# Kernel optimization log

Hardware: AMD Instinct MI355X
Metric: run time of the kernel (lower is better)

The kernel has to match this reference:

```python
import jax, jax.numpy as jnp
import numpy as np

NUM_NODES = 50000
NUM_EDGES = 800000
NUM_LABEL_EDGES = 100000
F_IN, F_HID, F_OUT = 128, 128, 64


def gcn_conv(x, src, dst, W, b, n):
    # PyG GCNConv: h = x @ W; add self-loops; symmetric normalization
    # deg counted on destination (col), including self-loop (+1).
    h = x @ W
    deg = jax.ops.segment_sum(jnp.ones(src.shape, h.dtype), dst, num_segments=n) + 1.0
    dinv = jax.lax.rsqrt(deg)  # deg >= 1 always (self-loop)
    norm = dinv[src] * dinv[dst]                       # [E]
    agg = jax.ops.segment_sum(h[src] * norm[:, None], dst, num_segments=n)
    agg = agg + h * (dinv * dinv)[:, None]             # self-loop term dinv[i]^2 * h[i]
    return agg + b


def setup_inputs() -> dict:
    key = jax.random.key(0)
    ks = jax.random.split(key, 9)
    x = jax.random.normal(ks[0], (NUM_NODES, F_IN), dtype=jnp.float32)
    edge_index = jax.random.randint(ks[1], (2, NUM_EDGES), 0, NUM_NODES, dtype=jnp.int64)
    edge_label_index = jax.random.randint(ks[2], (2, NUM_LABEL_EDGES), 0, NUM_NODES, dtype=jnp.int64)
    def glorot(k, fi, fo):
        s = (6.0 / (fi + fo)) ** 0.5
        return jax.random.uniform(k, (fi, fo), jnp.float32, -s, s)
    return {
        "x": x,
        "edge_index": edge_index,
        "edge_label_index": edge_label_index,
        "W1": glorot(ks[3], F_IN, F_HID),  "b1": jnp.zeros((F_HID,), jnp.float32),
        "W2": glorot(ks[4], F_HID, F_HID), "b2": jnp.zeros((F_HID,), jnp.float32),
        "W3": glorot(ks[5], F_HID, F_OUT), "b3": jnp.zeros((F_OUT,), jnp.float32),
    }


def reference(x, edge_index, edge_label_index, W1, b1, W2, b2, W3, b3):
    src, dst = edge_index[0], edge_index[1]
    z = jax.nn.relu(gcn_conv(x, src, dst, W1, b1, NUM_NODES))
    z = jax.nn.relu(gcn_conv(z, src, dst, W2, b2, NUM_NODES))
    z = gcn_conv(z, src, dst, W3, b3, NUM_NODES)
    # decode: dot product of endpoint embeddings per label edge
    return jnp.sum(z[edge_label_index[0]] * z[edge_label_index[1]], axis=-1)
```

## Files before the change

kernel.cpp:

```cpp
#include <hip/hip_runtime.h>
#include <hip/hip_bf16.h>
#include <stdint.h>

#define NN 50000
#define NE 800000
#define NL 100000
#define F_IN 128
#define F_HID 128
#define F_OUT 64
#define SLOTS 64

#define NB 196
#define BSH 8
#define BCAP 5376

typedef __attribute__((ext_vector_type(8))) short bf16x8;
typedef __attribute__((ext_vector_type(4))) float f32x4;
typedef __attribute__((ext_vector_type(4))) unsigned int u32x4;

__device__ __forceinline__ float asf(unsigned int u) {
    union { unsigned int i; float f; } c; c.i = u; return c.f;
}
__device__ __forceinline__ float bflo(unsigned int x) { return asf(x << 16); }
__device__ __forceinline__ float bfhi(unsigned int x) { return asf(x & 0xffff0000u); }
__device__ __forceinline__ unsigned short f2bf(float f) {
    union { float f; unsigned int i; } c; c.f = f;
    unsigned int u = c.i + (0x7fffu + ((c.i >> 16) & 1u));
    return (unsigned short)(u >> 16);
}


__global__ void wprep(const float* __restrict__ W1, const float* __restrict__ W2,
                      const float* __restrict__ W3, unsigned short* __restrict__ Wt,
                      int* __restrict__ cursor) {
    if (blockIdx.x == 0 && threadIdx.x < NB) cursor[threadIdx.x] = 0;
    int idx = blockIdx.x * 256 + threadIdx.x;
    const float* W; unsigned short* O; int base, Mloc;
    if (idx < 16384)      { W = W1; O = Wt;         base = idx;         Mloc = 128; }
    else if (idx < 32768) { W = W2; O = Wt + 16384; base = idx - 16384; Mloc = 128; }
    else                  { W = W3; O = Wt + 32768; base = idx - 32768; Mloc = 64;  }
    int n = base >> 7, k = base & 127;
    O[base] = f2bf(W[k * Mloc + n]);
}


__global__ __launch_bounds__(256) void bin_edges(
        const int* __restrict__ src, const int* __restrict__ dst,
        int* __restrict__ cursor, unsigned int* __restrict__ binbuf) {
    __shared__ int hcnt[NB];
    __shared__ int hbase[NB];
    int tid = threadIdx.x;
    if (tid < NB) hcnt[tid] = 0;
    __syncthreads();
    int e0 = blockIdx.x * 2048;
#pragma unroll
    for (int r = 0; r < 8; ++r) {
        int e = e0 + r * 256 + tid;
        if (e < NE) atomicAdd(&hcnt[dst[e] >> BSH], 1);
    }
    __syncthreads();
    if (tid < NB) { hbase[tid] = atomicAdd(&cursor[tid], hcnt[tid]); hcnt[tid] = 0; }
    __syncthreads();
#pragma unroll
    for (int r = 0; r < 8; ++r) {
        int e = e0 + r * 256 + tid;
        if (e < NE) {
            int d = dst[e], s = src[e];
            int b = d >> BSH;
            int p = hbase[b] + atomicAdd(&hcnt[b], 1);
            if (p < BCAP)
                __builtin_nontemporal_store(
                    (unsigned int)s | ((unsigned int)d << 16),
                    &binbuf[(size_t)b * BCAP + p]);
        }
    }
}


__global__ __launch_bounds__(256) void build_csr(
        const unsigned int* __restrict__ binbuf, const int* __restrict__ cursor,
        int* __restrict__ deg, unsigned short* __restrict__ colp) {
    __shared__ unsigned short lcol[256 * SLOTS];
    __shared__ int ldeg[256];
    int tid = threadIdx.x;
    int blk = blockIdx.x;
    int base = blk << BSH;
    int nNodes = min(256, NN - base);
    ldeg[tid] = 0;
    __syncthreads();
    int cnt = min(cursor[blk], BCAP);
    for (int e = tid; e < cnt; e += 256) {
        unsigned int pk = __builtin_nontemporal_load(&binbuf[(size_t)blk * BCAP + e]);
        int d = (int)(pk >> 16) - base;
        int p = atomicAdd(&ldeg[d], 1);
        if (p < SLOTS) lcol[d * SLOTS + p] = (unsigned short)(pk & 0xffffu);
    }
    __syncthreads();
    if (tid < nNodes) deg[base + tid] = ldeg[tid];
    u32x4* gout = (u32x4*)(colp + (size_t)base * SLOTS);
    const u32x4* lin = (const u32x4*)lcol;
    for (int i = tid; i < nNodes * 8; i += 256) gout[i] = lin[i];
}


template <int M_, int AFP32>
__global__ __launch_bounds__(256) void gemm_mfma(
        const void* __restrict__ Av, const unsigned short* __restrict__ Wt,
        const int* __restrict__ deg, unsigned short* __restrict__ Outb, int N) {
    constexpr int K = 128;
    constexpr int NT = M_ / 16;
    int lane = threadIdx.x & 63;
    int wave = threadIdx.x >> 6;
    int m    = lane & 15;
    int quad = lane >> 4;
    int rowA = blockIdx.x * 64 + wave * 16 + m;
    int rA   = min(rowA, N - 1);

    bf16x8 afr[4];
    if (AFP32) {
        const float* A = (const float*)Av;
        const float* p = A + (size_t)rA * K + quad * 8;
#pragma unroll
        for (int s = 0; s < 4; ++s) {
            float4 lo = *(const float4*)(p + s * 32);
            float4 hi = *(const float4*)(p + s * 32 + 4);
            bf16x8 r;
            r[0] = (short)f2bf(lo.x); r[1] = (short)f2bf(lo.y);
            r[2] = (short)f2bf(lo.z); r[3] = (short)f2bf(lo.w);
            r[4] = (short)f2bf(hi.x); r[5] = (short)f2bf(hi.y);
            r[6] = (short)f2bf(hi.z); r[7] = (short)f2bf(hi.w);
            afr[s] = r;
        }
    } else {
        const unsigned short* A = (const unsigned short*)Av;
#pragma unroll
        for (int s = 0; s < 4; ++s)
            afr[s] = *(const bf16x8*)(A + (size_t)rA * K + s * 32 + quad * 8);
    }

    f32x4 acc[NT];
#pragma unroll
    for (int t = 0; t < NT; ++t) { acc[t][0] = 0.f; acc[t][1] = 0.f; acc[t][2] = 0.f; acc[t][3] = 0.f; }

#pragma unroll
    for (int t = 0; t < NT; ++t) {
        const unsigned short* wp = Wt + (size_t)(t * 16 + m) * K + quad * 8;
#pragma unroll
        for (int s = 0; s < 4; ++s) {
            bf16x8 bfr = *(const bf16x8*)(wp + s * 32);
            acc[t] = __builtin_amdgcn_mfma_f32_16x16x32_bf16(afr[s], bfr, acc[t], 0, 0, 0);
        }
    }

    int outRowBase = blockIdx.x * 64 + wave * 16 + quad * 4;
    float di[4];
#pragma unroll
    for (int i = 0; i < 4; ++i) {
        int rr = min(outRowBase + i, N - 1);
        di[i] = rsqrtf((float)deg[rr] + 1.0f);
    }
#pragma unroll
    for (int t = 0; t < NT; ++t) {
#pragma unroll
        for (int i = 0; i < 4; ++i) {
            int rr = outRowBase + i;
            if (rr < N)
                Outb[(size_t)rr * M_ + t * 16 + m] = f2bf(acc[t][i] * di[i]);
        }
    }
}


template <int F, int RELU>
__global__ __launch_bounds__(256) void aggregate(
        const unsigned short* __restrict__ hs, const int* __restrict__ deg,
        const unsigned short* __restrict__ colp, const float* __restrict__ bias,
        unsigned short* __restrict__ out, int n) {
    int wave = threadIdx.x >> 6;
    int lane = threadIdx.x & 63;
    int node = blockIdx.x * 4 + wave;
    if (node >= n) return;

    float acc0 = 0.f, acc1 = 0.f;
    if (F == 128) {
        unsigned int v = *(const unsigned int*)(hs + (size_t)node * F + lane * 2);
        acc0 = bflo(v); acc1 = bfhi(v);
    } else {
        acc0 = bflo((unsigned int)hs[(size_t)node * F + lane]);
    }

    int cnt = min(deg[node], SLOTS);
    int myIdx = (lane < cnt) ? (int)colp[(size_t)node * SLOTS + lane] : 0;
    for (int j = 0; j < cnt; j += 8) {
        int iv[8]; unsigned int mk[8];
#pragma unroll
        for (int u = 0; u < 8; ++u) {
            iv[u] = __shfl(myIdx, j + u, 64);
            mk[u] = (j + u < cnt) ? 0xffffffffu : 0u;
        }
        if (F == 128) {
            unsigned int vv[8];
#pragma unroll
            for (int u = 0; u < 8; ++u)
                vv[u] = *(const unsigned int*)(hs + (size_t)iv[u] * F + lane * 2);
#pragma unroll
            for (int u = 0; u < 8; ++u) {
                unsigned int x = vv[u] & mk[u];
                acc0 += bflo(x); acc1 += bfhi(x);
            }
        } else {
            unsigned short vv[8];
#pragma unroll
            for (int u = 0; u < 8; ++u)
                vv[u] = hs[(size_t)iv[u] * F + lane];
#pragma unroll
            for (int u = 0; u < 8; ++u)
                acc0 += bflo(((unsigned int)vv[u]) & mk[u]);
        }
    }

    float di = rsqrtf((float)deg[node] + 1.0f);
    if (F == 128) {
        float o0 = di * acc0 + bias[lane * 2];
        float o1 = di * acc1 + bias[lane * 2 + 1];
        if (RELU) { o0 = fmaxf(o0, 0.f); o1 = fmaxf(o1, 0.f); }
        unsigned int w = (unsigned int)f2bf(o0) | ((unsigned int)f2bf(o1) << 16);
        *(unsigned int*)(out + (size_t)node * F + lane * 2) = w;
    } else {
        float o = di * acc0 + bias[lane];
        if (RELU) o = fmaxf(o, 0.f);
        out[(size_t)node * F + lane] = f2bf(o);
    }
}


__global__ __launch_bounds__(256) void decode(
        const unsigned short* __restrict__ z, const int* __restrict__ ls,
        const int* __restrict__ ld, float* __restrict__ out, int nl) {
    int wave = threadIdx.x >> 6;
    int lane = threadIdx.x & 63;
    int e = blockIdx.x * 4 + wave;
    if (e >= nl) return;
    float p = bflo((unsigned int)z[(size_t)ls[e] * F_OUT + lane]) *
              bflo((unsigned int)z[(size_t)ld[e] * F_OUT + lane]);
#pragma unroll
    for (int off = 32; off > 0; off >>= 1) p += __shfl_down(p, off, 64);
    if (lane == 0) out[e] = p;
}


static inline size_t align256(size_t x) { return (x + 255) & ~(size_t)255; }

extern "C" void kernel_launch(void* const* d_in, const int* in_sizes, int n_in,
                              void* d_out, int out_size, void* d_ws, size_t ws_size,
                              hipStream_t stream) {
    const float* x  = (const float*)d_in[0];
    const int*   ei = (const int*)d_in[1];
    const int*   li = (const int*)d_in[2];
    const float* W1 = (const float*)d_in[3];
    const float* b1 = (const float*)d_in[4];
    const float* W2 = (const float*)d_in[5];
    const float* b2 = (const float*)d_in[6];
    const float* W3 = (const float*)d_in[7];
    const float* b3 = (const float*)d_in[8];
    float* out = (float*)d_out;

    const int* src = ei;
    const int* dst = ei + NE;
    const int* ls = li;
    const int* ld = li + NL;

    char* ws = (char*)d_ws;
    size_t off = 0;
    int* deg    = (int*)(ws + off); off += align256(NN * 4);
    int* cursor = (int*)(ws + off); off += align256(NB * 4);
    unsigned int* binbuf = (unsigned int*)(ws + off); off += align256((size_t)NB * BCAP * 4);
    unsigned short* colp = (unsigned short*)(ws + off); off += align256((size_t)NN * SLOTS * 2);
    unsigned short* Wtb  = (unsigned short*)(ws + off); off += align256(40960 * 2);
    unsigned short* bufH = (unsigned short*)(ws + off); off += align256((size_t)NN * F_HID * 2);
    unsigned short* bufP = (unsigned short*)(ws + off); off += align256((size_t)NN * F_HID * 2);

    const int aggBlocks = (NN + 3) / 4;
    const int gemmBlocks = (NN + 63) / 64;
    const int binBlocks = (NE + 2047) / 2048;

    wprep<<<160, 256, 0, stream>>>(W1, W2, W3, Wtb, cursor);
    bin_edges<<<binBlocks, 256, 0, stream>>>(src, dst, cursor, binbuf);
    build_csr<<<NB, 256, 0, stream>>>(binbuf, cursor, deg, colp);

    gemm_mfma<128, 1><<<gemmBlocks, 256, 0, stream>>>(x, Wtb, deg, bufH, NN);
    aggregate<128, 1><<<aggBlocks, 256, 0, stream>>>(bufH, deg, colp, b1, bufP, NN);

    gemm_mfma<128, 0><<<gemmBlocks, 256, 0, stream>>>(bufP, Wtb + 16384, deg, bufH, NN);
    aggregate<128, 1><<<aggBlocks, 256, 0, stream>>>(bufH, deg, colp, b2, bufP, NN);

    gemm_mfma<64, 0><<<gemmBlocks, 256, 0, stream>>>(bufP, Wtb + 32768, deg, bufH, NN);
    aggregate<64, 0><<<aggBlocks, 256, 0, stream>>>(bufH, deg, colp, b3, bufP, NN);

    decode<<<(NL + 3) / 4, 256, 0, stream>>>(bufP, ls, ld, out, NL);
}
```

Measured before the change: 273.0 us.

## Fuse all stages into one persistent cooperative kernel with grid syncs

Replaces the ten separate kernel launches with a single cooperative persistent kernel. The kernel runs each stage (weight prep, edge binning, CSR build, three GEMM and aggregate pairs, decode) as grid-strided phases separated by grid.sync. The aim is to remove per-launch overhead and inter-kernel gaps. In exchange, each grid-wide barrier has a cost, occupancy is capped at 1024 blocks, and the phases lose the latency hiding that very large launches gave the aggregate stage. A fallback path with separate launches is kept for when the cooperative launch fails.

```diff
diff --git a/kernel.cpp b/kernel.cpp
--- a/kernel.cpp
+++ b/kernel.cpp
@@ -1,13 +1,13 @@
 #include <hip/hip_runtime.h>
+#include <hip/hip_cooperative_groups.h>
 #include <hip/hip_bf16.h>
 #include <stdint.h>
+
+namespace cg = cooperative_groups;
 
 #define NN 50000
 #define NE 800000
 #define NL 100000
-#define F_IN 128
-#define F_HID 128
-#define F_OUT 64
 #define SLOTS 64
 
 #define NB 196
@@ -30,222 +30,312 @@
 }
 
 
-__global__ void wprep(const float* __restrict__ W1, const float* __restrict__ W2,
-                      const float* __restrict__ W3, unsigned short* __restrict__ Wt,
-                      int* __restrict__ cursor) {
-    if (blockIdx.x == 0 && threadIdx.x < NB) cursor[threadIdx.x] = 0;
-    int idx = blockIdx.x * 256 + threadIdx.x;
-    const float* W; unsigned short* O; int base, Mloc;
-    if (idx < 16384)      { W = W1; O = Wt;         base = idx;         Mloc = 128; }
-    else if (idx < 32768) { W = W2; O = Wt + 16384; base = idx - 16384; Mloc = 128; }
-    else                  { W = W3; O = Wt + 32768; base = idx - 32768; Mloc = 64;  }
-    int n = base >> 7, k = base & 127;
-    O[base] = f2bf(W[k * Mloc + n]);
-}
-
-
-__global__ __launch_bounds__(256) void bin_edges(
+__device__ __forceinline__ void wprep_phase(
+        const float* __restrict__ W1, const float* __restrict__ W2,
+        const float* __restrict__ W3, unsigned short* __restrict__ Wt,
+        int* __restrict__ cursor) {
+    for (int idx = blockIdx.x * 256 + threadIdx.x; idx < 40960;
+         idx += gridDim.x * 256) {
+        if (idx < NB) cursor[idx] = 0;
+        const float* W; unsigned short* O; int base, Mloc;
+        if (idx < 16384)      { W = W1; O = Wt;         base = idx;         Mloc = 128; }
+        else if (idx < 32768) { W = W2; O = Wt + 16384; base = idx - 16384; Mloc = 128; }
+        else                  { W = W3; O = Wt + 32768; base = idx - 32768; Mloc = 64;  }
+        int n = base >> 7, k = base & 127;
+        O[base] = f2bf(W[k * Mloc + n]);
+    }
+}
+
+__device__ __forceinline__ void bin_phase(
+        const int* __restrict__ src, const int* __restrict__ dst,
+        int* __restrict__ cursor, unsigned int* __restrict__ binbuf,
+        int* hcnt, int* hbase) {
+    int tid = threadIdx.x;
+    if (tid < NB) hcnt[tid] = 0;
+    __syncthreads();
+    int chunk = (NE + gridDim.x - 1) / gridDim.x;
+    int e0 = blockIdx.x * chunk;
+    int e1 = min(e0 + chunk, NE);
+    for (int e = e0 + tid; e < e1; e += 256)
+        atomicAdd(&hcnt[dst[e] >> BSH], 1);
+    __syncthreads();
+    if (tid < NB) { hbase[tid] = atomicAdd(&cursor[tid], hcnt[tid]); hcnt[tid] = 0; }
+    __syncthreads();
+    for (int e = e0 + tid; e < e1; e += 256) {
+        int d = dst[e], s = src[e];
+        int b = d >> BSH;
+        int p = hbase[b] + atomicAdd(&hcnt[b], 1);
+        if (p < BCAP)
+            __builtin_nontemporal_store(
+                (unsigned int)s | ((unsigned int)d << 16),
+                &binbuf[(size_t)b * BCAP + p]);
+    }
+}
+
+__device__ __forceinline__ void csr_phase(
+        const unsigned int* __restrict__ binbuf, const int* __restrict__ cursor,
+        int* __restrict__ deg, unsigned short* __restrict__ colp,
+        unsigned short* lcol, int* ldeg) {
+    int tid = threadIdx.x;
+    for (int blk = blockIdx.x; blk < NB; blk += gridDim.x) {
+        int base = blk << BSH;
+        int nNodes = min(256, NN - base);
+        ldeg[tid] = 0;
+        __syncthreads();
+        int cnt = min(cursor[blk], BCAP);
+        for (int e = tid; e < cnt; e += 256) {
+            unsigned int pk = __builtin_nontemporal_load(&binbuf[(size_t)blk * BCAP + e]);
+            int d = (int)(pk >> 16) - base;
+            int p = atomicAdd(&ldeg[d], 1);
+            if (p < SLOTS) lcol[d * SLOTS + p] = (unsigned short)(pk & 0xffffu);
+        }
+        __syncthreads();
+        if (tid < nNodes) deg[base + tid] = ldeg[tid];
+        u32x4* gout = (u32x4*)(colp + (size_t)base * SLOTS);
+        const u32x4* lin = (const u32x4*)lcol;
+        for (int i = tid; i < nNodes * 8; i += 256) gout[i] = lin[i];
+        __syncthreads();
+    }
+}
+
+template <int M_, int AFP32>
+__device__ __forceinline__ void gemm_phase(
+        const void* __restrict__ Av, const unsigned short* __restrict__ Wt,
+        const int* __restrict__ deg, unsigned short* __restrict__ Outb, int N) {
+    constexpr int K = 128;
+    constexpr int NT = M_ / 16;
+    int tid = threadIdx.x;
+    int lane = tid & 63;
+    int wave = tid >> 6;
+    int m    = lane & 15;
+    int quad = lane >> 4;
+    const int VB = (NN + 63) / 64;
+    for (int vb = blockIdx.x; vb < VB; vb += gridDim.x) {
+        int rowA = vb * 64 + wave * 16 + m;
+        int rA   = min(rowA, N - 1);
+
+        bf16x8 afr[4];
+        if (AFP32) {
+            const float* A = (const float*)Av;
+            const float* p = A + (size_t)rA * K + quad * 8;
+#pragma unroll
+            for (int s = 0; s < 4; ++s) {
+                float4 lo = *(const float4*)(p + s * 32);
+                float4 hi = *(const float4*)(p + s * 32 + 4);
+                bf16x8 r;
+                r[0] = (short)f2bf(lo.x); r[1] = (short)f2bf(lo.y);
+                r[2] = (short)f2bf(lo.z); r[3] = (short)f2bf(lo.w);
+                r[4] = (short)f2bf(hi.x); r[5] = (short)f2bf(hi.y);
+                r[6] = (short)f2bf(hi.z); r[7] = (short)f2bf(hi.w);
+                afr[s] = r;
+            }
+        } else {
+            const unsigned short* A = (const unsigned short*)Av;
+#pragma unroll
+            for (int s = 0; s < 4; ++s)
+                afr[s] = *(const bf16x8*)(A + (size_t)rA * K + s * 32 + quad * 8);
+        }
+
+        f32x4 acc[NT];
+#pragma unroll
+        for (int t = 0; t < NT; ++t) { acc[t][0] = 0.f; acc[t][1] = 0.f; acc[t][2] = 0.f; acc[t][3] = 0.f; }
+
+#pragma unroll
+        for (int t = 0; t < NT; ++t) {
+            const unsigned short* wp = Wt + (size_t)(t * 16 + m) * K + quad * 8;
+#pragma unroll
+            for (int s = 0; s < 4; ++s) {
+                bf16x8 bfr = *(const bf16x8*)(wp + s * 32);
+                acc[t] = __builtin_amdgcn_mfma_f32_16x16x32_bf16(afr[s], bfr, acc[t], 0, 0, 0);
+            }
+        }
+
+        int outRowBase = vb * 64 + wave * 16 + quad * 4;
+        float di[4];
+#pragma unroll
+        for (int i = 0; i < 4; ++i) {
+            int rr = min(outRowBase + i, N - 1);
+            di[i] = rsqrtf((float)deg[rr] + 1.0f);
+        }
+#pragma unroll
+        for (int t = 0; t < NT; ++t) {
+#pragma unroll
+            for (int i = 0; i < 4; ++i) {
+                int rr = outRowBase + i;
+                if (rr < N)
+                    Outb[(size_t)rr * M_ + t * 16 + m] = f2bf(acc[t][i] * di[i]);
+            }
+        }
+    }
+}
+
+template <int F, int RELU>
+__device__ __forceinline__ void agg_phase(
+        const unsigned short* __restrict__ hs, const int* __restrict__ deg,
+        const unsigned short* __restrict__ colp, const float* __restrict__ bias,
+        unsigned short* __restrict__ out, int n) {
+    int tid = threadIdx.x;
+    int wave = tid >> 6;
+    int lane = tid & 63;
+    const int VB = (NN + 3) / 4;
+    for (int vb = blockIdx.x; vb < VB; vb += gridDim.x) {
+        int node = vb * 4 + wave;
+        if (node >= n) continue;
+
+        float acc0 = 0.f, acc1 = 0.f;
+        if (F == 128) {
+            unsigned int v = *(const unsigned int*)(hs + (size_t)node * F + lane * 2);
+            acc0 = bflo(v); acc1 = bfhi(v);
+        } else {
+            acc0 = bflo((unsigned int)hs[(size_t)node * F + lane]);
+        }
+
+        int cnt = min(deg[node], SLOTS);
+        int myIdx = (lane < cnt) ? (int)colp[(size_t)node * SLOTS + lane] : 0;
+        for (int j = 0; j < cnt; j += 8) {
+            int iv[8]; unsigned int mk[8];
+#pragma unroll
+            for (int u = 0; u < 8; ++u) {
+                iv[u] = __shfl(myIdx, j + u, 64);
+                mk[u] = (j + u < cnt) ? 0xffffffffu : 0u;
+            }
+            if (F == 128) {
+                unsigned int vv[8];
+#pragma unroll
+                for (int u = 0; u < 8; ++u)
+                    vv[u] = *(const unsigned int*)(hs + (size_t)iv[u] * F + lane * 2);
+#pragma unroll
+                for (int u = 0; u < 8; ++u) {
+                    unsigned int xv = vv[u] & mk[u];
+                    acc0 += bflo(xv); acc1 += bfhi(xv);
+                }
+            } else {
+                unsigned short vv[8];
+#pragma unroll
+                for (int u = 0; u < 8; ++u)
+                    vv[u] = hs[(size_t)iv[u] * F + lane];
+#pragma unroll
+                for (int u = 0; u < 8; ++u)
+                    acc0 += bflo(((unsigned int)vv[u]) & mk[u]);
+            }
+        }
+
+        float di = rsqrtf((float)deg[node] + 1.0f);
+        if (F == 128) {
+            float o0 = di * acc0 + bias[lane * 2];
+            float o1 = di * acc1 + bias[lane * 2 + 1];
+            if (RELU) { o0 = fmaxf(o0, 0.f); o1 = fmaxf(o1, 0.f); }
+            unsigned int w = (unsigned int)f2bf(o0) | ((unsigned int)f2bf(o1) << 16);
+            *(unsigned int*)(out + (size_t)node * F + lane * 2) = w;
+        } else {
+            float o = di * acc0 + bias[lane];
+            if (RELU) o = fmaxf(o, 0.f);
+            out[(size_t)node * F + lane] = f2bf(o);
+        }
+    }
+}
+
+__device__ __forceinline__ void decode_phase(
+        const unsigned short* __restrict__ z, const int* __restrict__ ls,
+        const int* __restrict__ ld, float* __restrict__ out) {
+    int tid = threadIdx.x;
+    int wave = tid >> 6;
+    int lane = tid & 63;
+    const int VB = (NL + 3) / 4;
+    for (int vb = blockIdx.x; vb < VB; vb += gridDim.x) {
+        int e = vb * 4 + wave;
+        if (e >= NL) continue;
+        float p = bflo((unsigned int)z[(size_t)ls[e] * 64 + lane]) *
+                  bflo((unsigned int)z[(size_t)ld[e] * 64 + lane]);
+#pragma unroll
+        for (int off = 32; off > 0; off >>= 1) p += __shfl_down(p, off, 64);
+        if (lane == 0) out[e] = p;
+    }
+}
+
+
+__global__ __launch_bounds__(256, 4) void fused(
+        const float* __restrict__ x, const int* __restrict__ ei,
+        const int* __restrict__ li,
+        const float* __restrict__ W1, const float* __restrict__ b1,
+        const float* __restrict__ W2, const float* __restrict__ b2,
+        const float* __restrict__ W3, const float* __restrict__ b3,
+        float* __restrict__ out,
+        int* __restrict__ deg, int* __restrict__ cursor,
+        unsigned int* __restrict__ binbuf, unsigned short* __restrict__ colp,
+        unsigned short* __restrict__ Wtb, unsigned short* __restrict__ bufH,
+        unsigned short* __restrict__ bufP) {
+    cg::grid_group grid = cg::this_grid();
+    __shared__ __align__(16) char smem[33792];
+    const int* src = ei;
+    const int* dst = ei + NE;
+
+    wprep_phase(W1, W2, W3, Wtb, cursor);
+    grid.sync();
+    bin_phase(src, dst, cursor, binbuf, (int*)smem, (int*)smem + NB);
+    grid.sync();
+    csr_phase(binbuf, cursor, deg, colp,
+              (unsigned short*)smem, (int*)(smem + 32768));
+    grid.sync();
+
+    gemm_phase<128, 1>(x, Wtb, deg, bufH, NN);
+    grid.sync();
+    agg_phase<128, 1>(bufH, deg, colp, b1, bufP, NN);
+    grid.sync();
+    gemm_phase<128, 0>(bufP, Wtb + 16384, deg, bufH, NN);
+    grid.sync();
+    agg_phase<128, 1>(bufH, deg, colp, b2, bufP, NN);
+    grid.sync();
+    gemm_phase<64, 0>(bufP, Wtb + 32768, deg, bufH, NN);
+    grid.sync();
+    agg_phase<64, 0>(bufH, deg, colp, b3, bufP, NN);
+    grid.sync();
+
+    decode_phase(bufP, li, li + NL, out);
+}
+
+
+__global__ void k_wprep(const float* __restrict__ W1, const float* __restrict__ W2,
+                        const float* __restrict__ W3, unsigned short* __restrict__ Wt,
+                        int* __restrict__ cursor) {
+    wprep_phase(W1, W2, W3, Wt, cursor);
+}
+
+__global__ __launch_bounds__(256) void k_bin(
         const int* __restrict__ src, const int* __restrict__ dst,
         int* __restrict__ cursor, unsigned int* __restrict__ binbuf) {
     __shared__ int hcnt[NB];
     __shared__ int hbase[NB];
-    int tid = threadIdx.x;
-    if (tid < NB) hcnt[tid] = 0;
-    __syncthreads();
-    int e0 = blockIdx.x * 2048;
-#pragma unroll
-    for (int r = 0; r < 8; ++r) {
-        int e = e0 + r * 256 + tid;
-        if (e < NE) atomicAdd(&hcnt[dst[e] >> BSH], 1);
-    }
-    __syncthreads();
-    if (tid < NB) { hbase[tid] = atomicAdd(&cursor[tid], hcnt[tid]); hcnt[tid] = 0; }
-    __syncthreads();
-#pragma unroll
-    for (int r = 0; r < 8; ++r) {
-        int e = e0 + r * 256 + tid;
-        if (e < NE) {
-            int d = dst[e], s = src[e];
-            int b = d >> BSH;
-            int p = hbase[b] + atomicAdd(&hcnt[b], 1);
-            if (p < BCAP)
-                __builtin_nontemporal_store(
-                    (unsigned int)s | ((unsigned int)d << 16),
-                    &binbuf[(size_t)b * BCAP + p]);
-        }
-    }
-}
-
-
-__global__ __launch_bounds__(256) void build_csr(
+    bin_phase(src, dst, cursor, binbuf, hcnt, hbase);
+}
+
+__global__ __launch_bounds__(256) void k_csr(
         const unsigned int* __restrict__ binbuf, const int* __restrict__ cursor,
         int* __restrict__ deg, unsigned short* __restrict__ colp) {
     __shared__ unsigned short lcol[256 * SLOTS];
     __shared__ int ldeg[256];
-    int tid = threadIdx.x;
-    int blk = blockIdx.x;
-    int base = blk << BSH;
-    int nNodes = min(256, NN - base);
-    ldeg[tid] = 0;
-    __syncthreads();
-    int cnt = min(cursor[blk], BCAP);
-    for (int e = tid; e < cnt; e += 256) {
-        unsigned int pk = __builtin_nontemporal_load(&binbuf[(size_t)blk * BCAP + e]);
-        int d = (int)(pk >> 16) - base;
-        int p = atomicAdd(&ldeg[d], 1);
-        if (p < SLOTS) lcol[d * SLOTS + p] = (unsigned short)(pk & 0xffffu);
-    }
-    __syncthreads();
-    if (tid < nNodes) deg[base + tid] = ldeg[tid];
-    u32x4* gout = (u32x4*)(colp + (size_t)base * SLOTS);
-    const u32x4* lin = (const u32x4*)lcol;
-    for (int i = tid; i < nNodes * 8; i += 256) gout[i] = lin[i];
-}
-
+    csr_phase(binbuf, cursor, deg, colp, lcol, ldeg);
+}
 
 template <int M_, int AFP32>
-__global__ __launch_bounds__(256) void gemm_mfma(
+__global__ __launch_bounds__(256) void k_gemm(
         const void* __restrict__ Av, const unsigned short* __restrict__ Wt,
         const int* __restrict__ deg, unsigned short* __restrict__ Outb, int N) {
-    constexpr int K = 128;
-    constexpr int NT = M_ / 16;
-    int lane = threadIdx.x & 63;
-    int wave = threadIdx.x >> 6;
-    int m    = lane & 15;
-    int quad = lane >> 4;
-    int rowA = blockIdx.x * 64 + wave * 16 + m;
-    int rA   = min(rowA, N - 1);
-
-    bf16x8 afr[4];
-    if (AFP32) {
-        const float* A = (const float*)Av;
-        const float* p = A + (size_t)rA * K + quad * 8;
-#pragma unroll
-        for (int s = 0; s < 4; ++s) {
-            float4 lo = *(const float4*)(p + s * 32);
-            float4 hi = *(const float4*)(p + s * 32 + 4);
-            bf16x8 r;
-            r[0] = (short)f2bf(lo.x); r[1] = (short)f2bf(lo.y);
-            r[2] = (short)f2bf(lo.z); r[3] = (short)f2bf(lo.w);
-            r[4] = (short)f2bf(hi.x); r[5] = (short)f2bf(hi.y);
-            r[6] = (short)f2bf(hi.z); r[7] = (short)f2bf(hi.w);
-            afr[s] = r;
-        }
-    } else {
-        const unsigned short* A = (const unsigned short*)Av;
-#pragma unroll
-        for (int s = 0; s < 4; ++s)
-            afr[s] = *(const bf16x8*)(A + (size_t)rA * K + s * 32 + quad * 8);
-    }
-
-    f32x4 acc[NT];
-#pragma unroll
-    for (int t = 0; t < NT; ++t) { acc[t][0] = 0.f; acc[t][1] = 0.f; acc[t][2] = 0.f; acc[t][3] = 0.f; }
-
-#pragma unroll
-    for (int t = 0; t < NT; ++t) {
-        const unsigned short* wp = Wt + (size_t)(t * 16 + m) * K + quad * 8;
-#pragma unroll
-        for (int s = 0; s < 4; ++s) {
-            bf16x8 bfr = *(const bf16x8*)(wp + s * 32);
-            acc[t] = __builtin_amdgcn_mfma_f32_16x16x32_bf16(afr[s], bfr, acc[t], 0, 0, 0);
-        }
-    }
-
-    int outRowBase = blockIdx.x * 64 + wave * 16 + quad * 4;
-    float di[4];
-#pragma unroll
-    for (int i = 0; i < 4; ++i) {
-        int rr = min(outRowBase + i, N - 1);
-        di[i] = rsqrtf((float)deg[rr] + 1.0f);
-    }
-#pragma unroll
-    for (int t = 0; t < NT; ++t) {
-#pragma unroll
-        for (int i = 0; i < 4; ++i) {
-            int rr = outRowBase + i;
-            if (rr < N)
-                Outb[(size_t)rr * M_ + t * 16 + m] = f2bf(acc[t][i] * di[i]);
-        }
-    }
-}
-
+    gemm_phase<M_, AFP32>(Av, Wt, deg, Outb, N);
+}
 
 template <int F, int RELU>
-__global__ __launch_bounds__(256) void aggregate(
+__global__ __launch_bounds__(256) void k_agg(
         const unsigned short* __restrict__ hs, const int* __restrict__ deg,
         const unsigned short* __restrict__ colp, const float* __restrict__ bias,
         unsigned short* __restrict__ out, int n) {
-    int wave = threadIdx.x >> 6;
-    int lane = threadIdx.x & 63;
-    int node = blockIdx.x * 4 + wave;
-    if (node >= n) return;
-
-    float acc0 = 0.f, acc1 = 0.f;
-    if (F == 128) {
-        unsigned int v = *(const unsigned int*)(hs + (size_t)node * F + lane * 2);
-        acc0 = bflo(v); acc1 = bfhi(v);
-    } else {
-        acc0 = bflo((unsigned int)hs[(size_t)node * F + lane]);
-    }
-
-    int cnt = min(deg[node], SLOTS);
-    int myIdx = (lane < cnt) ? (int)colp[(size_t)node * SLOTS + lane] : 0;
-    for (int j = 0; j < cnt; j += 8) {
-        int iv[8]; unsigned int mk[8];
-#pragma unroll
-        for (int u = 0; u < 8; ++u) {
-            iv[u] = __shfl(myIdx, j + u, 64);
-            mk[u] = (j + u < cnt) ? 0xffffffffu : 0u;
-        }
-        if (F == 128) {
-            unsigned int vv[8];
-#pragma unroll
-            for (int u = 0; u < 8; ++u)
-                vv[u] = *(const unsigned int*)(hs + (size_t)iv[u] * F + lane * 2);
-#pragma unroll
-            for (int u = 0; u < 8; ++u) {
-                unsigned int x = vv[u] & mk[u];
-                acc0 += bflo(x); acc1 += bfhi(x);
-            }
-        } else {
-            unsigned short vv[8];
-#pragma unroll
-            for (int u = 0; u < 8; ++u)
-                vv[u] = hs[(size_t)iv[u] * F + lane];
-#pragma unroll
-            for (int u = 0; u < 8; ++u)
-                acc0 += bflo(((unsigned int)vv[u]) & mk[u]);
-        }
-    }
-
-    float di = rsqrtf((float)deg[node] + 1.0f);
-    if (F == 128) {
-        float o0 = di * acc0 + bias[lane * 2];
-        float o1 = di * acc1 + bias[lane * 2 + 1];
-        if (RELU) { o0 = fmaxf(o0, 0.f); o1 = fmaxf(o1, 0.f); }
-        unsigned int w = (unsigned int)f2bf(o0) | ((unsigned int)f2bf(o1) << 16);
-        *(unsigned int*)(out + (size_t)node * F + lane * 2) = w;
-    } else {
-        float o = di * acc0 + bias[lane];
-        if (RELU) o = fmaxf(o, 0.f);
-        out[(size_t)node * F + lane] = f2bf(o);
-    }
-}
-
-
-__global__ __launch_bounds__(256) void decode(
+    agg_phase<F, RELU>(hs, deg, colp, bias, out, n);
+}
+
+__global__ __launch_bounds__(256) void k_decode(
         const unsigned short* __restrict__ z, const int* __restrict__ ls,
-        const int* __restrict__ ld, float* __restrict__ out, int nl) {
-    int wave = threadIdx.x >> 6;
-    int lane = threadIdx.x & 63;
-    int e = blockIdx.x * 4 + wave;
-    if (e >= nl) return;
-    float p = bflo((unsigned int)z[(size_t)ls[e] * F_OUT + lane]) *
-              bflo((unsigned int)z[(size_t)ld[e] * F_OUT + lane]);
-#pragma unroll
-    for (int off = 32; off > 0; off >>= 1) p += __shfl_down(p, off, 64);
-    if (lane == 0) out[e] = p;
+        const int* __restrict__ ld, float* __restrict__ out) {
+    decode_phase(z, ls, ld, out);
 }
 
 
@@ -265,11 +355,6 @@
     const float* b3 = (const float*)d_in[8];
     float* out = (float*)d_out;
 
-    const int* src = ei;
-    const int* dst = ei + NE;
-    const int* ls = li;
-    const int* ld = li + NL;
-
     char* ws = (char*)d_ws;
     size_t off = 0;
     int* deg    = (int*)(ws + off); off += align256(NN * 4);
@@ -277,25 +362,39 @@
     unsigned int* binbuf = (unsigned int*)(ws + off); off += align256((size_t)NB * BCAP * 4);
     unsigned short* colp = (unsigned short*)(ws + off); off += align256((size_t)NN * SLOTS * 2);
     unsigned short* Wtb  = (unsigned short*)(ws + off); off += align256(40960 * 2);
-    unsigned short* bufH = (unsigned short*)(ws + off); off += align256((size_t)NN * F_HID * 2);
-    unsigned short* bufP = (unsigned short*)(ws + off); off += align256((size_t)NN * F_HID * 2);
-
-    const int aggBlocks = (NN + 3) / 4;
-    const int gemmBlocks = (NN + 63) / 64;
-    const int binBlocks = (NE + 2047) / 2048;
-
-    wprep<<<160, 256, 0, stream>>>(W1, W2, W3, Wtb, cursor);
-    bin_edges<<<binBlocks, 256, 0, stream>>>(src, dst, cursor, binbuf);
-    build_csr<<<NB, 256, 0, stream>>>(binbuf, cursor, deg, colp);
-
-    gemm_mfma<128, 1><<<gemmBlocks, 256, 0, stream>>>(x, Wtb, deg, bufH, NN);
-    aggregate<128, 1><<<aggBlocks, 256, 0, stream>>>(bufH, deg, colp, b1, bufP, NN);
-
-    gemm_mfma<128, 0><<<gemmBlocks, 256, 0, stream>>>(bufP, Wtb + 16384, deg, bufH, NN);
-    aggregate<128, 1><<<aggBlocks, 256, 0, stream>>>(bufH, deg, colp, b2, bufP, NN);
-
-    gemm_mfma<64, 0><<<gemmBlocks, 256, 0, stream>>>(bufP, Wtb + 32768, deg, bufH, NN);
-    aggregate<64, 0><<<aggBlocks, 256, 0, stream>>>(bufH, deg, colp, b3, bufP, NN);
-
-    decode<<<(NL + 3) / 4, 256, 0, stream>>>(bufP, ls, ld, out, NL);
-}
+    unsigned short* bufH = (unsigned short*)(ws + off); off += align256((size_t)NN * 128 * 2);
+    unsigned short* bufP = (unsigned short*)(ws + off); off += align256((size_t)NN * 128 * 2);
+
+    int perCU = 0;
+    hipError_t oe = hipOccupancyMaxActiveBlocksPerMultiprocessor(&perCU, fused, 256, 0);
+    bool coop_ok = false;
+    if (oe == hipSuccess && perCU > 0) {
+        int grid = perCU * 256;
+        if (grid > 1024) grid = 1024;
+        void* kargs[] = {
+            (void*)&x, (void*)&ei, (void*)&li,
+            (void*)&W1, (void*)&b1, (void*)&W2, (void*)&b2, (void*)&W3, (void*)&b3,
+            (void*)&out,
+            (void*)&deg, (void*)&cursor, (void*)&binbuf, (void*)&colp,
+            (void*)&Wtb, (void*)&bufH, (void*)&bufP
+        };
+        hipError_t le = hipLaunchCooperativeKernel((const void*)fused, dim3(grid),
+                                                   dim3(256), kargs, 0, stream);
+        coop_ok = (le == hipSuccess);
+    }
+
+    if (!coop_ok) {
+        const int* src = ei;
+        const int* dst = ei + NE;
+        k_wprep<<<160, 256, 0, stream>>>(W1, W2, W3, Wtb, cursor);
+        k_bin<<<391, 256, 0, stream>>>(src, dst, cursor, binbuf);
+        k_csr<<<NB, 256, 0, stream>>>(binbuf, cursor, deg, colp);
+        k_gemm<128, 1><<<782, 256, 0, stream>>>(x, Wtb, deg, bufH, NN);
+        k_agg<128, 1><<<12500, 256, 0, stream>>>(bufH, deg, colp, b1, bufP, NN);
+        k_gemm<128, 0><<<782, 256, 0, stream>>>(bufP, Wtb + 16384, deg, bufH, NN);
+        k_agg<128, 1><<<12500, 256, 0, stream>>>(bufH, deg, colp, b2, bufP, NN);
+        k_gemm<64, 0><<<782, 256, 0, stream>>>(bufP, Wtb + 32768, deg, bufH, NN);
+        k_agg<64, 0><<<12500, 256, 0, stream>>>(bufH, deg, colp, b3, bufP, NN);
+        k_decode<<<25000, 256, 0, stream>>>(bufP, li, li + NL, out);
+    }
+}
```

New measurement: 931.1 us. 241% more time.

## Fuse aggregation of layers 1-2 with the following GEMM via LDS tiles

Applied to the files above, without the earlier changes.

Each block of the new kernel aggregates 16 nodes' neighbor features, applies bias, ReLU and normalization, and stages the bf16 rows in shared memory. The block then runs the next layer's MFMA GEMM on that tile directly. This removes two global write/read round trips of the hidden activations and two kernel launches. In exchange each block covers only 16 rows and reloads the full weight matrix from cache, which lowers GEMM efficiency. Other edits are renames and specialization of templates into fixed kernels.

```diff
diff --git a/kernel.cpp b/kernel.cpp
--- a/kernel.cpp
+++ b/kernel.cpp
@@ -5,9 +5,6 @@
 #define NN 50000
 #define NE 800000
 #define NL 100000
-#define F_IN 128
-#define F_HID 128
-#define F_OUT 64
 #define SLOTS 64
 
 #define NB 196
@@ -29,12 +26,11 @@
     return (unsigned short)(u >> 16);
 }
 
-
-__global__ void wprep(const float* __restrict__ W1, const float* __restrict__ W2,
-                      const float* __restrict__ W3, unsigned short* __restrict__ Wt,
-                      int* __restrict__ cursor) {
-    if (blockIdx.x == 0 && threadIdx.x < NB) cursor[threadIdx.x] = 0;
+__global__ void k_wprep(const float* __restrict__ W1, const float* __restrict__ W2,
+                        const float* __restrict__ W3, unsigned short* __restrict__ Wt,
+                        int* __restrict__ cursor) {
     int idx = blockIdx.x * 256 + threadIdx.x;
+    if (idx < NB) cursor[idx] = 0;
     const float* W; unsigned short* O; int base, Mloc;
     if (idx < 16384)      { W = W1; O = Wt;         base = idx;         Mloc = 128; }
     else if (idx < 32768) { W = W2; O = Wt + 16384; base = idx - 16384; Mloc = 128; }
@@ -43,8 +39,7 @@
     O[base] = f2bf(W[k * Mloc + n]);
 }
 
-
-__global__ __launch_bounds__(256) void bin_edges(
+__global__ __launch_bounds__(256) void k_bin(
         const int* __restrict__ src, const int* __restrict__ dst,
         int* __restrict__ cursor, unsigned int* __restrict__ binbuf) {
     __shared__ int hcnt[NB];
@@ -53,31 +48,24 @@
     if (tid < NB) hcnt[tid] = 0;
     __syncthreads();
     int e0 = blockIdx.x * 2048;
-#pragma unroll
-    for (int r = 0; r < 8; ++r) {
-        int e = e0 + r * 256 + tid;
-        if (e < NE) atomicAdd(&hcnt[dst[e] >> BSH], 1);
-    }
+    int e1 = min(e0 + 2048, NE);
+    for (int e = e0 + tid; e < e1; e += 256)
+        atomicAdd(&hcnt[dst[e] >> BSH], 1);
     __syncthreads();
     if (tid < NB) { hbase[tid] = atomicAdd(&cursor[tid], hcnt[tid]); hcnt[tid] = 0; }
     __syncthreads();
-#pragma unroll
-    for (int r = 0; r < 8; ++r) {
-        int e = e0 + r * 256 + tid;
-        if (e < NE) {
-            int d = dst[e], s = src[e];
-            int b = d >> BSH;
-            int p = hbase[b] + atomicAdd(&hcnt[b], 1);
-            if (p < BCAP)
-                __builtin_nontemporal_store(
-                    (unsigned int)s | ((unsigned int)d << 16),
-                    &binbuf[(size_t)b * BCAP + p]);
-        }
-    }
-}
-
-
-__global__ __launch_bounds__(256) void build_csr(
+    for (int e = e0 + tid; e < e1; e += 256) {
+        int d = dst[e], s = src[e];
+        int b = d >> BSH;
+        int p = hbase[b] + atomicAdd(&hcnt[b], 1);
+        if (p < BCAP)
+            __builtin_nontemporal_store(
+                (unsigned int)s | ((unsigned int)d << 16),
+                &binbuf[(size_t)b * BCAP + p]);
+    }
+}
+
+__global__ __launch_bounds__(256) void k_csr(
         const unsigned int* __restrict__ binbuf, const int* __restrict__ cursor,
         int* __restrict__ deg, unsigned short* __restrict__ colp) {
     __shared__ unsigned short lcol[256 * SLOTS];
@@ -102,46 +90,34 @@
     for (int i = tid; i < nNodes * 8; i += 256) gout[i] = lin[i];
 }
 
-
-template <int M_, int AFP32>
-__global__ __launch_bounds__(256) void gemm_mfma(
-        const void* __restrict__ Av, const unsigned short* __restrict__ Wt,
+__global__ __launch_bounds__(256) void k_gemm1(
+        const float* __restrict__ A, const unsigned short* __restrict__ Wt,
         const int* __restrict__ deg, unsigned short* __restrict__ Outb, int N) {
     constexpr int K = 128;
-    constexpr int NT = M_ / 16;
-    int lane = threadIdx.x & 63;
-    int wave = threadIdx.x >> 6;
-    int m    = lane & 15;
-    int quad = lane >> 4;
+    constexpr int NT = 8;
+    int tid = threadIdx.x;
+    int lane = tid & 63, wave = tid >> 6;
+    int m = lane & 15, quad = lane >> 4;
     int rowA = blockIdx.x * 64 + wave * 16 + m;
-    int rA   = min(rowA, N - 1);
+    int rA = min(rowA, N - 1);
 
     bf16x8 afr[4];
-    if (AFP32) {
-        const float* A = (const float*)Av;
-        const float* p = A + (size_t)rA * K + quad * 8;
-#pragma unroll
-        for (int s = 0; s < 4; ++s) {
-            float4 lo = *(const float4*)(p + s * 32);
-            float4 hi = *(const float4*)(p + s * 32 + 4);
-            bf16x8 r;
-            r[0] = (short)f2bf(lo.x); r[1] = (short)f2bf(lo.y);
-            r[2] = (short)f2bf(lo.z); r[3] = (short)f2bf(lo.w);
-            r[4] = (short)f2bf(hi.x); r[5] = (short)f2bf(hi.y);
-            r[6] = (short)f2bf(hi.z); r[7] = (short)f2bf(hi.w);
-            afr[s] = r;
-        }
-    } else {
-        const unsigned short* A = (const unsigned short*)Av;
-#pragma unroll
-        for (int s = 0; s < 4; ++s)
-            afr[s] = *(const bf16x8*)(A + (size_t)rA * K + s * 32 + quad * 8);
+    const float* p = A + (size_t)rA * K + quad * 8;
+#pragma unroll
+    for (int s = 0; s < 4; ++s) {
+        float4 lo = *(const float4*)(p + s * 32);
+        float4 hi = *(const float4*)(p + s * 32 + 4);
+        bf16x8 r;
+        r[0] = (short)f2bf(lo.x); r[1] = (short)f2bf(lo.y);
+        r[2] = (short)f2bf(lo.z); r[3] = (short)f2bf(lo.w);
+        r[4] = (short)f2bf(hi.x); r[5] = (short)f2bf(hi.y);
+        r[6] = (short)f2bf(hi.z); r[7] = (short)f2bf(hi.w);
+        afr[s] = r;
     }
 
     f32x4 acc[NT];
 #pragma unroll
     for (int t = 0; t < NT; ++t) { acc[t][0] = 0.f; acc[t][1] = 0.f; acc[t][2] = 0.f; acc[t][3] = 0.f; }
-
 #pragma unroll
     for (int t = 0; t < NT; ++t) {
         const unsigned short* wp = Wt + (size_t)(t * 16 + m) * K + quad * 8;
@@ -155,40 +131,105 @@
     int outRowBase = blockIdx.x * 64 + wave * 16 + quad * 4;
     float di[4];
 #pragma unroll
-    for (int i = 0; i < 4; ++i) {
-        int rr = min(outRowBase + i, N - 1);
-        di[i] = rsqrtf((float)deg[rr] + 1.0f);
-    }
-#pragma unroll
-    for (int t = 0; t < NT; ++t) {
+    for (int i = 0; i < 4; ++i) di[i] = rsqrtf((float)deg[min(outRowBase + i, N - 1)] + 1.0f);
+#pragma unroll
+    for (int t = 0; t < NT; ++t)
 #pragma unroll
         for (int i = 0; i < 4; ++i) {
             int rr = outRowBase + i;
-            if (rr < N)
-                Outb[(size_t)rr * M_ + t * 16 + m] = f2bf(acc[t][i] * di[i]);
-        }
-    }
-}
-
-
-template <int F, int RELU>
-__global__ __launch_bounds__(256) void aggregate(
+            if (rr < N) Outb[(size_t)rr * 128 + t * 16 + m] = f2bf(acc[t][i] * di[i]);
+        }
+}
+
+template <int M_>
+__global__ __launch_bounds__(256) void k_agg_gemm(
+        const unsigned short* __restrict__ hs, const int* __restrict__ deg,
+        const unsigned short* __restrict__ colp, const float* __restrict__ bias,
+        const unsigned short* __restrict__ Wt, unsigned short* __restrict__ Outb) {
+    constexpr int K = 128;
+    constexpr int NT = M_ / 64;
+    __shared__ unsigned short As[16][132];
+    int tid = threadIdx.x;
+    int lane = tid & 63, wave = tid >> 6;
+    int tileBase = blockIdx.x * 16;
+
+#pragma unroll
+    for (int t = 0; t < 4; ++t) {
+        int r = wave * 4 + t;
+        int node = tileBase + r;
+        unsigned int v = *(const unsigned int*)(hs + (size_t)node * K + lane * 2);
+        float acc0 = bflo(v), acc1 = bfhi(v);
+
+        int cnt = min(deg[node], SLOTS);
+        int myIdx = (lane < cnt) ? (int)colp[(size_t)node * SLOTS + lane] : 0;
+        for (int j = 0; j < cnt; j += 8) {
+            int iv[8]; unsigned int mk[8];
+#pragma unroll
+            for (int u = 0; u < 8; ++u) {
+                iv[u] = __shfl(myIdx, j + u, 64);
+                mk[u] = (j + u < cnt) ? 0xffffffffu : 0u;
+            }
+            unsigned int vv[8];
+#pragma unroll
+            for (int u = 0; u < 8; ++u)
+                vv[u] = *(const unsigned int*)(hs + (size_t)iv[u] * K + lane * 2);
+#pragma unroll
+            for (int u = 0; u < 8; ++u) {
+                unsigned int xv = vv[u] & mk[u];
+                acc0 += bflo(xv); acc1 += bfhi(xv);
+            }
+        }
+        float di = rsqrtf((float)deg[node] + 1.0f);
+        float o0 = fmaxf(di * acc0 + bias[lane * 2], 0.f);
+        float o1 = fmaxf(di * acc1 + bias[lane * 2 + 1], 0.f);
+        *(unsigned int*)&As[r][lane * 2] =
+            (unsigned int)f2bf(o0) | ((unsigned int)f2bf(o1) << 16);
+    }
+    __syncthreads();
+
+    int m = lane & 15, quad = lane >> 4;
+    bf16x8 afr[4];
+#pragma unroll
+    for (int s = 0; s < 4; ++s)
+        afr[s] = *(const bf16x8*)&As[m][s * 32 + quad * 8];
+
+    f32x4 acc[NT];
+#pragma unroll
+    for (int t = 0; t < NT; ++t) { acc[t][0] = 0.f; acc[t][1] = 0.f; acc[t][2] = 0.f; acc[t][3] = 0.f; }
+#pragma unroll
+    for (int t = 0; t < NT; ++t) {
+        int ct = wave * NT + t;
+        const unsigned short* wp = Wt + (size_t)(ct * 16 + m) * K + quad * 8;
+#pragma unroll
+        for (int s = 0; s < 4; ++s) {
+            bf16x8 bfr = *(const bf16x8*)(wp + s * 32);
+            acc[t] = __builtin_amdgcn_mfma_f32_16x16x32_bf16(afr[s], bfr, acc[t], 0, 0, 0);
+        }
+    }
+
+    int rowBase = tileBase + quad * 4;
+    float di[4];
+#pragma unroll
+    for (int i = 0; i < 4; ++i) di[i] = rsqrtf((float)deg[rowBase + i] + 1.0f);
+#pragma unroll
+    for (int t = 0; t < NT; ++t) {
+        int ct = wave * NT + t;
+#pragma unroll
+        for (int i = 0; i < 4; ++i)
+            Outb[(size_t)(rowBase + i) * M_ + ct * 16 + m] = f2bf(acc[t][i] * di[i]);
+    }
+}
+
+__global__ __launch_bounds__(256) void k_agg64(
         const unsigned short* __restrict__ hs, const int* __restrict__ deg,
         const unsigned short* __restrict__ colp, const float* __restrict__ bias,
         unsigned short* __restrict__ out, int n) {
-    int wave = threadIdx.x >> 6;
-    int lane = threadIdx.x & 63;
+    int tid = threadIdx.x;
+    int wave = tid >> 6, lane = tid & 63;
     int node = blockIdx.x * 4 + wave;
     if (node >= n) return;
 
-    float acc0 = 0.f, acc1 = 0.f;
-    if (F == 128) {
-        unsigned int v = *(const unsigned int*)(hs + (size_t)node * F + lane * 2);
-        acc0 = bflo(v); acc1 = bfhi(v);
-    } else {
-        acc0 = bflo((unsigned int)hs[(size_t)node * F + lane]);
-    }
-
+    float acc0 = bflo((unsigned int)hs[(size_t)node * 64 + lane]);
     int cnt = min(deg[node], SLOTS);
     int myIdx = (lane < cnt) ? (int)colp[(size_t)node * SLOTS + lane] : 0;
     for (int j = 0; j < cnt; j += 8) {
@@ -198,51 +239,27 @@
             iv[u] = __shfl(myIdx, j + u, 64);
             mk[u] = (j + u < cnt) ? 0xffffffffu : 0u;
         }
-        if (F == 128) {
-            unsigned int vv[8];
-#pragma unroll
-            for (int u = 0; u < 8; ++u)
-                vv[u] = *(const unsigned int*)(hs + (size_t)iv[u] * F + lane * 2);
-#pragma unroll
-            for (int u = 0; u < 8; ++u) {
-                unsigned int x = vv[u] & mk[u];
-                acc0 += bflo(x); acc1 += bfhi(x);
-            }
-        } else {
-            unsigned short vv[8];
-#pragma unroll
-            for (int u = 0; u < 8; ++u)
-                vv[u] = hs[(size_t)iv[u] * F + lane];
-#pragma unroll
-            for (int u = 0; u < 8; ++u)
-                acc0 += bflo(((unsigned int)vv[u]) & mk[u]);
-        }
-    }
-
+        unsigned short vv[8];
+#pragma unroll
+        for (int u = 0; u < 8; ++u)
+            vv[u] = hs[(size_t)iv[u] * 64 + lane];
+#pragma unroll
+        for (int u = 0; u < 8; ++u)
+            acc0 += bflo(((unsigned int)vv[u]) & mk[u]);
+    }
     float di = rsqrtf((float)deg[node] + 1.0f);
-    if (F == 128) {
-        float o0 = di * acc0 + bias[lane * 2];
-        float o1 = di * acc1 + bias[lane * 2 + 1];
-        if (RELU) { o0 = fmaxf(o0, 0.f); o1 = fmaxf(o1, 0.f); }
-        unsigned int w = (unsigned int)f2bf(o0) | ((unsigned int)f2bf(o1) << 16);
-        *(unsigned int*)(out + (size_t)node * F + lane * 2) = w;
-    } else {
-        float o = di * acc0 + bias[lane];
-        if (RELU) o = fmaxf(o, 0.f);
-        out[(size_t)node * F + lane] = f2bf(o);
-    }
-}
-
-
-__global__ __launch_bounds__(256) void decode(
+    out[(size_t)node * 64 + lane] = f2bf(di * acc0 + bias[lane]);
+}
+
+__global__ __launch_bounds__(256) void k_decode(
         const unsigned short* __restrict__ z, const int* __restrict__ ls,
         const int* __restrict__ ld, float* __restrict__ out, int nl) {
     int wave = threadIdx.x >> 6;
     int lane = threadIdx.x & 63;
     int e = blockIdx.x * 4 + wave;
     if (e >= nl) return;
-    float p = bflo((unsigned int)z[(size_t)ls[e] * F_OUT + lane]) *
-              bflo((unsigned int)z[(size_t)ld[e] * F_OUT + lane]);
+    float p = bflo((unsigned int)z[(size_t)ls[e] * 64 + lane]) *
+              bflo((unsigned int)z[(size_t)ld[e] * 64 + lane]);
 #pragma unroll
     for (int off = 32; off > 0; off >>= 1) p += __shfl_down(p, off, 64);
     if (lane == 0) out[e] = p;
@@ -277,25 +294,17 @@
     unsigned int* binbuf = (unsigned int*)(ws + off); off += align256((size_t)NB * BCAP * 4);
     unsigned short* colp = (unsigned short*)(ws + off); off += align256((size_t)NN * SLOTS * 2);
     unsigned short* Wtb  = (unsigned short*)(ws + off); off += align256(40960 * 2);
-    unsigned short* bufH = (unsigned short*)(ws + off); off += align256((size_t)NN * F_HID * 2);
-    unsigned short* bufP = (unsigned short*)(ws + off); off += align256((size_t)NN * F_HID * 2);
-
-    const int aggBlocks = (NN + 3) / 4;
-    const int gemmBlocks = (NN + 63) / 64;
-    const int binBlocks = (NE + 2047) / 2048;
-
-    wprep<<<160, 256, 0, stream>>>(W1, W2, W3, Wtb, cursor);
-    bin_edges<<<binBlocks, 256, 0, stream>>>(src, dst, cursor, binbuf);
-    build_csr<<<NB, 256, 0, stream>>>(binbuf, cursor, deg, colp);
-
-    gemm_mfma<128, 1><<<gemmBlocks, 256, 0, stream>>>(x, Wtb, deg, bufH, NN);
-    aggregate<128, 1><<<aggBlocks, 256, 0, stream>>>(bufH, deg, colp, b1, bufP, NN);
-
-    gemm_mfma<128, 0><<<gemmBlocks, 256, 0, stream>>>(bufP, Wtb + 16384, deg, bufH, NN);
-    aggregate<128, 1><<<aggBlocks, 256, 0, stream>>>(bufH, deg, colp, b2, bufP, NN);
-
-    gemm_mfma<64, 0><<<gemmBlocks, 256, 0, stream>>>(bufP, Wtb + 32768, deg, bufH, NN);
-    aggregate<64, 0><<<aggBlocks, 256, 0, stream>>>(bufH, deg, colp, b3, bufP, NN);
-
-    decode<<<(NL + 3) / 4, 256, 0, stream>>>(bufP, ls, ld, out, NL);
-}
+    unsigned short* bufA = (unsigned short*)(ws + off); off += align256((size_t)NN * 128 * 2);
+    unsigned short* bufB = (unsigned short*)(ws + off); off += align256((size_t)NN * 128 * 2);
+    unsigned short* bufZ = (unsigned short*)(ws + off); off += align256((size_t)NN * 64 * 2);
+
+    k_wprep<<<160, 256, 0, stream>>>(W1, W2, W3, Wtb, cursor);
+    k_bin<<<391, 256, 0, stream>>>(src, dst, cursor, binbuf);
+    k_csr<<<NB, 256, 0, stream>>>(binbuf, cursor, deg, colp);
+
+    k_gemm1<<<782, 256, 0, stream>>>(x, Wtb, deg, bufA, NN);
+    k_agg_gemm<128><<<3125, 256, 0, stream>>>(bufA, deg, colp, b1, Wtb + 16384, bufB);
+    k_agg_gemm<64><<<3125, 256, 0, stream>>>(bufB, deg, colp, b2, Wtb + 32768, bufA);
+    k_agg64<<<12500, 256, 0, stream>>>(bufA, deg, colp, b3, bufZ, NN);
+    k_decode<<<25000, 256, 0, stream>>>(bufZ, ls, ld, out, NL);
+}
```

Result: faster. 250.2 us (-8.4%).
